# Kernel optimization log

Measured on AMD Instinct MI355X. Metric: run time of the kernel, lower is better.

The kernel has to match this reference:

```python
import jax, jax.numpy as jnp
import numpy as np

DIMS = (2000, 500, 400)
H, DK, DV = 8, 32, 32
DM = H * DV  # 256
NUM_CLASS = 5
BS = 16384
TEMP = DK ** 0.5
LN_EPS = 1e-6


def setup_inputs() -> dict:
    key = jax.random.key(0)
    ks = jax.random.split(key, 32)
    inp = {"input_data": jax.random.normal(ks[0], (BS, sum(DIMS)), dtype=jnp.float32)}
    i = 1
    for name, odim in (("q", H * DK), ("k", H * DK), ("v", H * DV)):
        for m, d in enumerate(DIMS):
            inp[f"w{name}{m}"] = jax.random.normal(ks[i], (d, odim), dtype=jnp.float32) * (1.0 / np.sqrt(d)); i += 1
            inp[f"b{name}{m}"] = jnp.zeros((odim,), dtype=jnp.float32)
    inp["fc_w"] = jax.random.normal(ks[i], (DM, DM), dtype=jnp.float32) * (1.0 / np.sqrt(DM)); i += 1
    inp["fc_b"] = jnp.zeros((DM,), dtype=jnp.float32)
    inp["ln_g"] = jnp.ones((DM,), dtype=jnp.float32)
    inp["ln_b"] = jnp.zeros((DM,), dtype=jnp.float32)
    inp["out_w"] = jax.random.normal(ks[i], (len(DIMS) * DM, NUM_CLASS), dtype=jnp.float32) * (1.0 / np.sqrt(len(DIMS) * DM)); i += 1
    inp["out_b"] = jnp.zeros((NUM_CLASS,), dtype=jnp.float32)
    return inp


def _forward(input_data, wq, bq, wk, bk, wv, bv, fc_w, fc_b, ln_g, ln_b, out_w, out_b):
    bs = input_data.shape[0]
    M = len(DIMS)
    offs = np.concatenate([[0], np.cumsum(DIMS)])
    xs = [input_data[:, offs[m]:offs[m + 1]] for m in range(M)]
    # per-modality projections -> [bs, M, H*D]
    q = jnp.stack([xs[m] @ wq[m] + bq[m] for m in range(M)], axis=1)
    k = jnp.stack([xs[m] @ wk[m] + bk[m] for m in range(M)], axis=1)
    v = jnp.stack([xs[m] @ wv[m] + bv[m] for m in range(M)], axis=1)
    # [bs, H, M, D]
    qh = q.reshape(bs, M, H, DK).transpose(0, 2, 1, 3)
    kh = k.reshape(bs, M, H, DK).transpose(0, 2, 1, 3)
    vh = v.reshape(bs, M, H, DV).transpose(0, 2, 1, 3)
    attn = jnp.einsum("bhmd,bhnd->bhmn", qh / TEMP, kh)
    attn = attn / jnp.abs(attn.min())  # global-min scaling as in source
    attn = attn / jnp.maximum(jnp.sum(jnp.abs(attn), axis=-1, keepdims=True), 1e-12)  # L1 normalize
    attn = jax.nn.softmax(attn, axis=-1)
    o = jnp.einsum("bhmn,bhnd->bhmd", attn, vh)
    o = o.transpose(0, 2, 1, 3).reshape(bs, M, DM)
    residual = v  # [bs, M, DM]
    o = o @ fc_w + fc_b
    x = o + residual
    mu = x.mean(axis=-1, keepdims=True)
    var = ((x - mu) ** 2).mean(axis=-1, keepdims=True)
    x = (x - mu) / jnp.sqrt(var + LN_EPS) * ln_g + ln_b
    return x.reshape(bs, -1) @ out_w + out_b


def reference(input_data, wq0, bq0, wq1, bq1, wq2, bq2, wk0, bk0, wk1, bk1, wk2, bk2,
              wv0, bv0, wv1, bv1, wv2, bv2, fc_w, fc_b, ln_g, ln_b, out_w, out_b):
    return _forward(input_data, (wq0, wq1, wq2), (bq0, bq1, bq2), (wk0, wk1, wk2), (bk0, bk1, bk2),
                    (wv0, wv1, wv2), (bv0, bv1, bv2), fc_w, fc_b, ln_g, ln_b, out_w, out_b)
```

## Files before the change

kernel.cpp:

```cpp
#include <hip/hip_runtime.h>
#include <hip/hip_bf16.h>

#define BATCH 16384
#define HEADS 8
#define DDK 32
#define NQKV 768
#define NCLASS 5
#define LN_EPS 1e-6f

#define BM 128
#define BN 128
#define BKK 32

typedef short bf16x8 __attribute__((ext_vector_type(8)));
typedef float f32x4 __attribute__((ext_vector_type(4)));

__device__ __forceinline__ unsigned short f2bf(float x) {
    unsigned u = __float_as_uint(x);
    u += 0x7fff + ((u >> 16) & 1);
    return (unsigned short)(u >> 16);
}
__device__ __forceinline__ float bf2f(unsigned short b) {
    return __uint_as_float(((unsigned)b) << 16);
}

__device__ __forceinline__ void gl16(const unsigned short* g, unsigned short* l) {
    __builtin_amdgcn_global_load_lds(
        (const __attribute__((address_space(1))) unsigned int*)g,
        (__attribute__((address_space(3))) unsigned int*)l, 16, 0, 0);
}

__global__ __launch_bounds__(256) void convert_x(const float* __restrict__ X,
                                                 unsigned short* __restrict__ A,
                                                 int Kdim, int Kpad, int xoff,
                                                 int r0, int nrows) {
    const int k8n = Kpad >> 3;
    const int total = nrows * k8n;
    for (int i = blockIdx.x * blockDim.x + threadIdx.x; i < total;
         i += gridDim.x * blockDim.x) {
        const int rl = i / k8n;
        const int k8 = (i - rl * k8n) << 3;
        const float* src = X + (size_t)(r0 + rl) * 2900 + xoff + k8;
        float xv[8];
        if (k8 + 8 <= Kdim) {
            float4 v0 = *reinterpret_cast<const float4*>(src);
            float4 v1 = *reinterpret_cast<const float4*>(src + 4);
            xv[0] = v0.x; xv[1] = v0.y; xv[2] = v0.z; xv[3] = v0.w;
            xv[4] = v1.x; xv[5] = v1.y; xv[6] = v1.z; xv[7] = v1.w;
        } else {
#pragma unroll
            for (int j = 0; j < 8; ++j) xv[j] = (k8 + j < Kdim) ? src[j] : 0.f;
        }
        union { unsigned short s[8]; uint4 v; } hi, lo;
#pragma unroll
        for (int j = 0; j < 8; ++j) {
            hi.s[j] = f2bf(xv[j]);
            lo.s[j] = f2bf(xv[j] - bf2f(hi.s[j]));
        }
        unsigned short* dst = A + (size_t)rl * (2 * Kpad) + k8;
        *reinterpret_cast<uint4*>(dst) = hi.v;
        *reinterpret_cast<uint4*>(dst + Kpad) = lo.v;
    }
}

__global__ __launch_bounds__(256) void convert_w(
    const float* __restrict__ wq, const float* __restrict__ wk,
    const float* __restrict__ wv, const float* __restrict__ bq,
    const float* __restrict__ bk, const float* __restrict__ bv,
    unsigned short* __restrict__ Bt, float* __restrict__ bias,
    int Kdim, int Kpad) {
    const int gid0 = blockIdx.x * blockDim.x + threadIdx.x;
    if (gid0 < NQKV) {
        const int p = gid0 >> 8, c = gid0 & 255;
        bias[gid0] = (p == 0 ? bq : p == 1 ? bk : bv)[c];
    }
    const int k8n = Kpad >> 3;
    const int total = NQKV * k8n;
    for (int i = gid0; i < total; i += gridDim.x * blockDim.x) {
        const int kb = i / NQKV;
        const int n = i - kb * NQKV;
        const int k8 = kb << 3;
        const int p = n >> 8, c = n & 255;
        const float* wsrc = (p == 0 ? wq : p == 1 ? wk : wv);
        union { unsigned short s[8]; uint4 v; } hi, lo;
#pragma unroll
        for (int j = 0; j < 8; ++j) {
            float x = (k8 + j < Kdim) ? wsrc[(size_t)(k8 + j) * 256 + c] : 0.f;
            hi.s[j] = f2bf(x);
            lo.s[j] = f2bf(x - bf2f(hi.s[j]));
        }
        unsigned short* dst = Bt + (size_t)n * (2 * Kpad) + k8;
        *reinterpret_cast<uint4*>(dst) = hi.v;
        *reinterpret_cast<uint4*>(dst + Kpad) = lo.v;
    }
}

__global__ __launch_bounds__(256) void qkv_mfma(
    const unsigned short* __restrict__ A,
    const unsigned short* __restrict__ Bt,
    const float* __restrict__ bias,
    float* __restrict__ Qo, float* __restrict__ Ko, float* __restrict__ Vo,
    int Kpad, int mz, int r0) {
    const int ld = 2 * Kpad;
    const int row0l = blockIdx.x * BM;
    const int nb = blockIdx.y * BN;
    const int tid = threadIdx.x;
    const int lane = tid & 63;
    const int w = tid >> 6;
    const int wr = w >> 1, wc = w & 1;

    __shared__ alignas(16) unsigned short AsH[BM * BKK];
    __shared__ alignas(16) unsigned short AsL[BM * BKK];
    __shared__ alignas(16) unsigned short BsH[BN * BKK];
    __shared__ alignas(16) unsigned short BsL[BN * BKK];

    f32x4 acc[4][4];
#pragma unroll
    for (int i = 0; i < 4; ++i)
#pragma unroll
        for (int j = 0; j < 4; ++j) acc[i][j] = (f32x4){0.f, 0.f, 0.f, 0.f};

    const int rs = lane >> 2;
    const int kk = (lane & 3) * 8;
    const size_t gA0 = (size_t)(row0l + w * 16 + rs) * ld + kk;
    const size_t gA1 = (size_t)(row0l + (w + 4) * 16 + rs) * ld + kk;
    const size_t gB0 = (size_t)(nb + w * 16 + rs) * ld + kk;
    const size_t gB1 = (size_t)(nb + (w + 4) * 16 + rs) * ld + kk;
    unsigned short* lAH0 = &AsH[w * 512];
    unsigned short* lAH1 = &AsH[(w + 4) * 512];
    unsigned short* lAL0 = &AsL[w * 512];
    unsigned short* lAL1 = &AsL[(w + 4) * 512];
    unsigned short* lBH0 = &BsH[w * 512];
    unsigned short* lBH1 = &BsH[(w + 4) * 512];
    unsigned short* lBL0 = &BsL[w * 512];
    unsigned short* lBL1 = &BsL[(w + 4) * 512];

    const int fr = lane & 15;
    const int fk = (lane >> 4) * 8;
    const int aoff0 = (wr * 64 + fr) * BKK + fk;
    const int boff0 = (wc * 64 + fr) * BKK + fk;

    const int nk = Kpad >> 5;
#pragma unroll 1
    for (int kt = 0; kt < nk; ++kt) {
        const int k0 = kt * BKK;
        __syncthreads();
        gl16(A + gA0 + k0, lAH0);
        gl16(A + gA1 + k0, lAH1);
        gl16(A + Kpad + gA0 + k0, lAL0);
        gl16(A + Kpad + gA1 + k0, lAL1);
        gl16(Bt + gB0 + k0, lBH0);
        gl16(Bt + gB1 + k0, lBH1);
        gl16(Bt + Kpad + gB0 + k0, lBL0);
        gl16(Bt + Kpad + gB1 + k0, lBL1);
        __syncthreads();

        bf16x8 ah[4], bh[4];
#pragma unroll
        for (int mi = 0; mi < 4; ++mi)
            ah[mi] = *reinterpret_cast<const bf16x8*>(&AsH[aoff0 + mi * 16 * BKK]);
#pragma unroll
        for (int ni = 0; ni < 4; ++ni)
            bh[ni] = *reinterpret_cast<const bf16x8*>(&BsH[boff0 + ni * 16 * BKK]);
#pragma unroll
        for (int mi = 0; mi < 4; ++mi)
#pragma unroll
            for (int ni = 0; ni < 4; ++ni)
                acc[mi][ni] = __builtin_amdgcn_mfma_f32_16x16x32_bf16(
                    ah[mi], bh[ni], acc[mi][ni], 0, 0, 0);
        {
            bf16x8 al[4];
#pragma unroll
            for (int mi = 0; mi < 4; ++mi)
                al[mi] = *reinterpret_cast<const bf16x8*>(&AsL[aoff0 + mi * 16 * BKK]);
#pragma unroll
            for (int mi = 0; mi < 4; ++mi)
#pragma unroll
                for (int ni = 0; ni < 4; ++ni)
                    acc[mi][ni] = __builtin_amdgcn_mfma_f32_16x16x32_bf16(
                        al[mi], bh[ni], acc[mi][ni], 0, 0, 0);
        }
        {
            bf16x8 bl[4];
#pragma unroll
            for (int ni = 0; ni < 4; ++ni)
                bl[ni] = *reinterpret_cast<const bf16x8*>(&BsL[boff0 + ni * 16 * BKK]);
#pragma unroll
            for (int mi = 0; mi < 4; ++mi)
#pragma unroll
                for (int ni = 0; ni < 4; ++ni)
                    acc[mi][ni] = __builtin_amdgcn_mfma_f32_16x16x32_bf16(
                        ah[mi], bl[ni], acc[mi][ni], 0, 0, 0);
        }
    }

#pragma unroll
    for (int ni = 0; ni < 4; ++ni) {
        const int gc = nb + wc * 64 + ni * 16 + fr;
        const int proj = gc >> 8;
        const int col = gc & 255;
        const float bv = bias[gc];
        float* outp = (proj == 0 ? Qo : proj == 1 ? Ko : Vo);
#pragma unroll
        for (int mi = 0; mi < 4; ++mi) {
            const int gr = r0 + row0l + wr * 64 + mi * 16 + (lane >> 4) * 4;
            float* p = outp + (size_t)gr * NQKV + mz * 256 + col;
#pragma unroll
            for (int j = 0; j < 4; ++j)
                p[(size_t)j * NQKV] = acc[mi][ni][j] + bv;
        }
    }
}

__global__ __launch_bounds__(256) void attn_kernel(const float* __restrict__ Q,
                                                   const float* __restrict__ K,
                                                   const float* __restrict__ V,
                                                   float* __restrict__ O) {
    const int s = blockIdx.x;
    const int t = threadIdx.x;
    __shared__ float qs[NQKV], ks[NQKV], vs[NQKV];
    __shared__ float att[HEADS][3][3];

    const size_t base = (size_t)s * NQKV;
    for (int i = t; i < NQKV; i += 256) {
        qs[i] = Q[base + i];
        ks[i] = K[base + i];
        vs[i] = V[base + i];
    }
    __syncthreads();

    if (t < 72) {
        const int h = t / 9, ij = t % 9, i = ij / 3, j = ij % 3;
        const float* qp = &qs[i * 256 + h * 32];
        const float* kp = &ks[j * 256 + h * 32];
        float sc = 0.f;
#pragma unroll
        for (int d = 0; d < DDK; ++d) sc = fmaf(qp[d], kp[d], sc);
        att[h][i][j] = sc;
    }
    __syncthreads();
    if (t < 24) {
        const int h = t / 3, i = t % 3;
        float s0 = att[h][i][0], s1 = att[h][i][1], s2 = att[h][i][2];
        float r = fabsf(s0) + fabsf(s1) + fabsf(s2);
        r = fmaxf(r, 1e-12f);
        float p0 = s0 / r, p1 = s1 / r, p2 = s2 / r;
        float mx = fmaxf(p0, fmaxf(p1, p2));
        float e0 = expf(p0 - mx), e1 = expf(p1 - mx), e2 = expf(p2 - mx);
        float inv = 1.f / (e0 + e1 + e2);
        att[h][i][0] = e0 * inv;
        att[h][i][1] = e1 * inv;
        att[h][i][2] = e2 * inv;
    }
    __syncthreads();

    const int c = t;
    const int h = c >> 5;
#pragma unroll
    for (int m = 0; m < 3; ++m) {
        float o = att[h][m][0] * vs[c] + att[h][m][1] * vs[256 + c] + att[h][m][2] * vs[512 + c];
        O[base + m * 256 + c] = o;
    }
}

__global__ __launch_bounds__(256) void fc_gemm(const float* __restrict__ A,
                                               const float* __restrict__ W,
                                               const float* __restrict__ bias,
                                               const float* __restrict__ resid,
                                               float* __restrict__ X) {
    const int row0 = blockIdx.x * BM;
    const int nbase = blockIdx.y * BN;

    __shared__ float As[BKK][BM + 4];
    __shared__ float Bs[BKK][BN + 4];

    const int tid = threadIdx.x;
    const int tx = tid & 15;
    const int ty = tid >> 4;

    float acc[8][8];
#pragma unroll
    for (int i = 0; i < 8; ++i)
#pragma unroll
        for (int j = 0; j < 8; ++j) acc[i][j] = 0.f;

    for (int k0 = 0; k0 < 256; k0 += BKK) {
        {
            const int r = tid >> 3;
            const int kq = (tid & 7) * 4;
#pragma unroll
            for (int it = 0; it < 4; ++it) {
                const int row = r + it * 32;
                float4 v = *reinterpret_cast<const float4*>(
                    &A[(size_t)(row0 + row) * 256 + k0 + kq]);
                As[kq + 0][row] = v.x;
                As[kq + 1][row] = v.y;
                As[kq + 2][row] = v.z;
                As[kq + 3][row] = v.w;
            }
        }
        {
            const int kkk = tid >> 5;
            const int n4 = (tid & 31) * 4;
#pragma unroll
            for (int it = 0; it < 4; ++it) {
                const int krow = kkk + it * 8;
                *reinterpret_cast<float4*>(&Bs[krow][n4]) =
                    *reinterpret_cast<const float4*>(&W[(size_t)(k0 + krow) * 256 + nbase + n4]);
            }
        }
        __syncthreads();
#pragma unroll 8
        for (int k = 0; k < BKK; ++k) {
            float4 a0 = *reinterpret_cast<float4*>(&As[k][ty * 4]);
            float4 a1 = *reinterpret_cast<float4*>(&As[k][ty * 4 + 64]);
            float4 b0 = *reinterpret_cast<float4*>(&Bs[k][tx * 4]);
            float4 b1 = *reinterpret_cast<float4*>(&Bs[k][tx * 4 + 64]);
            float av[8] = {a0.x, a0.y, a0.z, a0.w, a1.x, a1.y, a1.z, a1.w};
            float bv[8] = {b0.x, b0.y, b0.z, b0.w, b1.x, b1.y, b1.z, b1.w};
#pragma unroll
            for (int i = 0; i < 8; ++i)
#pragma unroll
                for (int j = 0; j < 8; ++j)
                    acc[i][j] = fmaf(av[i], bv[j], acc[i][j]);
        }
        __syncthreads();
    }

#pragma unroll
    for (int rh = 0; rh < 2; ++rh) {
#pragma unroll
        for (int i = 0; i < 4; ++i) {
            const int row = row0 + rh * 64 + ty * 4 + i;
#pragma unroll
            for (int ch = 0; ch < 2; ++ch) {
                const int c = ch * 64 + tx * 4;
                const size_t off = (size_t)row * 256 + nbase + c;
                float4 rv = *reinterpret_cast<const float4*>(&resid[off]);
                float4 o;
                o.x = acc[rh * 4 + i][ch * 4 + 0] + bias[nbase + c + 0] + rv.x;
                o.y = acc[rh * 4 + i][ch * 4 + 1] + bias[nbase + c + 1] + rv.y;
                o.z = acc[rh * 4 + i][ch * 4 + 2] + bias[nbase + c + 2] + rv.z;
                o.w = acc[rh * 4 + i][ch * 4 + 3] + bias[nbase + c + 3] + rv.w;
                *reinterpret_cast<float4*>(&X[off]) = o;
            }
        }
    }
}

__global__ __launch_bounds__(256) void ln_out_kernel(const float* __restrict__ X,
                                                     const float* __restrict__ g,
                                                     const float* __restrict__ bb,
                                                     const float* __restrict__ ow,
                                                     const float* __restrict__ ob,
                                                     float* __restrict__ out) {
    const int s = blockIdx.x;
    const int t = threadIdx.x;
    const int lane = t & 63, wv = t >> 6;
    __shared__ float xr[NQKV];
    __shared__ float red1[4], red2[4];
    __shared__ float cpart[4][NCLASS];

    const size_t base = (size_t)s * NQKV;
    const float gg = g[t];
    const float bbv = bb[t];

    for (int m = 0; m < 3; ++m) {
        float v = X[base + m * 256 + t];
        float s1 = v, s2 = v * v;
#pragma unroll
        for (int off = 32; off > 0; off >>= 1) {
            s1 += __shfl_down(s1, off);
            s2 += __shfl_down(s2, off);
        }
        if (lane == 0) { red1[wv] = s1; red2[wv] = s2; }
        __syncthreads();
        const float tot = red1[0] + red1[1] + red1[2] + red1[3];
        const float tot2 = red2[0] + red2[1] + red2[2] + red2[3];
        const float mu = tot * (1.f / 256.f);
        const float var = tot2 * (1.f / 256.f) - mu * mu;
        const float inv = 1.0f / sqrtf(var + LN_EPS);
        xr[m * 256 + t] = (v - mu) * inv * gg + bbv;
        __syncthreads();
    }

    float p[NCLASS] = {0.f, 0.f, 0.f, 0.f, 0.f};
    for (int i = t; i < NQKV; i += 256) {
        const float xv = xr[i];
#pragma unroll
        for (int c = 0; c < NCLASS; ++c) p[c] = fmaf(xv, ow[i * NCLASS + c], p[c]);
    }
#pragma unroll
    for (int c = 0; c < NCLASS; ++c) {
        float pv = p[c];
#pragma unroll
        for (int off = 32; off > 0; off >>= 1) pv += __shfl_down(pv, off);
        if (lane == 0) cpart[wv][c] = pv;
    }
    __syncthreads();
    if (t < NCLASS)
        out[(size_t)s * NCLASS + t] =
            cpart[0][t] + cpart[1][t] + cpart[2][t] + cpart[3][t] + ob[t];
}

extern "C" void kernel_launch(void* const* d_in, const int* in_sizes, int n_in,
                              void* d_out, int out_size, void* d_ws, size_t ws_size,
                              hipStream_t stream) {
    const float* x = (const float*)d_in[0];
    const float* wq[3] = {(const float*)d_in[1], (const float*)d_in[3], (const float*)d_in[5]};
    const float* bq[3] = {(const float*)d_in[2], (const float*)d_in[4], (const float*)d_in[6]};
    const float* wk[3] = {(const float*)d_in[7], (const float*)d_in[9], (const float*)d_in[11]};
    const float* bk[3] = {(const float*)d_in[8], (const float*)d_in[10], (const float*)d_in[12]};
    const float* wvv[3] = {(const float*)d_in[13], (const float*)d_in[15], (const float*)d_in[17]};
    const float* bv[3] = {(const float*)d_in[14], (const float*)d_in[16], (const float*)d_in[18]};
    const float* fc_w = (const float*)d_in[19];
    const float* fc_b = (const float*)d_in[20];
    const float* ln_g = (const float*)d_in[21];
    const float* ln_b = (const float*)d_in[22];
    const float* out_w = (const float*)d_in[23];
    const float* out_b = (const float*)d_in[24];

    float* ws = (float*)d_ws;
    const size_t SZ = (size_t)BATCH * NQKV;
    float* Q = ws;
    float* Kb = ws + SZ;
    float* Vb = ws + 2 * SZ;
    float* biasx = ws + 3 * SZ;
    unsigned short* Bt = (unsigned short*)(biasx + NQKV);
    unsigned short* Aext = Bt + (size_t)NQKV * 4096;

    const size_t fixed_bytes = (3 * SZ + NQKV) * sizeof(float) +
                               (size_t)NQKV * 4096 * sizeof(unsigned short);
    size_t avail = (ws_size > fixed_bytes) ? ws_size - fixed_bytes : 0;
    size_t rc = (avail / (4096 * sizeof(unsigned short))) & ~(size_t)127;
    if (rc < 128) rc = 128;
    if (rc > BATCH) rc = BATCH;
    const int rows_chunk = (int)rc;

    float* O = Kb;
    float* X = Q;

    const int Kdim[3] = {2000, 500, 400};
    const int Kpad[3] = {2048, 512, 448};
    const int xoff[3] = {0, 2000, 2500};

    for (int m = 0; m < 3; ++m) {
        convert_w<<<768, 256, 0, stream>>>(wq[m], wk[m], wvv[m], bq[m], bk[m], bv[m],
                                           Bt, biasx, Kdim[m], Kpad[m]);
        for (int r0 = 0; r0 < BATCH; r0 += rows_chunk) {
            const int nr = (BATCH - r0 < rows_chunk) ? (BATCH - r0) : rows_chunk;
            const int cgrid = ((nr * (Kpad[m] >> 3)) + 255) / 256;
            convert_x<<<(cgrid < 2048 ? cgrid : 2048), 256, 0, stream>>>(
                x, Aext, Kdim[m], Kpad[m], xoff[m], r0, nr);
            dim3 g(nr / BM, NQKV / BN);
            qkv_mfma<<<g, 256, 0, stream>>>(Aext, Bt, biasx, Q, Kb, Vb, Kpad[m], m, r0);
        }
    }

    attn_kernel<<<BATCH, 256, 0, stream>>>(Q, Kb, Vb, O);

    dim3 g3((BATCH * 3) / BM, 2);
    fc_gemm<<<g3, 256, 0, stream>>>(O, fc_w, fc_b, Vb, X);

    ln_out_kernel<<<BATCH, 256, 0, stream>>>(X, ln_g, ln_b, out_w, out_b, (float*)d_out);
}
```

Baseline: 804.3 us.

## Switch split-precision GEMMs to fp16 with single-term weights and MFMA fc layer

Replaces the bf16 hi/lo three-product emulation in the QKV GEMM with fp16: activations stay split into hi/lo, but weights are rounded to a single fp16 term. This removes one third of the MFMA work and one of the LDS tile loads per K step. The scalar fp32 fc GEMM becomes an fp16 MFMA kernel whose attention output is split into hi/lo halves. Weight conversion for all three modalities and the fc layer is merged into one launch, and row chunks are sized per modality. The risk is accuracy: fp16 weights carry only 11 bits of mantissa, and fp16 range could overflow.

```diff
diff --git a/kernel.cpp b/kernel.cpp
--- a/kernel.cpp
+++ b/kernel.cpp
@@ -12,26 +12,17 @@
 #define BN 128
 #define BKK 32
 
-typedef short bf16x8 __attribute__((ext_vector_type(8)));
+typedef _Float16 f16x8 __attribute__((ext_vector_type(8)));
 typedef float f32x4 __attribute__((ext_vector_type(4)));
 
-__device__ __forceinline__ unsigned short f2bf(float x) {
-    unsigned u = __float_as_uint(x);
-    u += 0x7fff + ((u >> 16) & 1);
-    return (unsigned short)(u >> 16);
-}
-__device__ __forceinline__ float bf2f(unsigned short b) {
-    return __uint_as_float(((unsigned)b) << 16);
-}
-
-__device__ __forceinline__ void gl16(const unsigned short* g, unsigned short* l) {
+__device__ __forceinline__ void gl16(const void* g, void* l) {
     __builtin_amdgcn_global_load_lds(
         (const __attribute__((address_space(1))) unsigned int*)g,
         (__attribute__((address_space(3))) unsigned int*)l, 16, 0, 0);
 }
 
 __global__ __launch_bounds__(256) void convert_x(const float* __restrict__ X,
-                                                 unsigned short* __restrict__ A,
+                                                 _Float16* __restrict__ A,
                                                  int Kdim, int Kpad, int xoff,
                                                  int r0, int nrows) {
     const int k8n = Kpad >> 3;
@@ -51,53 +42,71 @@
 #pragma unroll
             for (int j = 0; j < 8; ++j) xv[j] = (k8 + j < Kdim) ? src[j] : 0.f;
         }
-        union { unsigned short s[8]; uint4 v; } hi, lo;
+        union { _Float16 h[8]; uint4 v; } hi, lo;
 #pragma unroll
         for (int j = 0; j < 8; ++j) {
-            hi.s[j] = f2bf(xv[j]);
-            lo.s[j] = f2bf(xv[j] - bf2f(hi.s[j]));
-        }
-        unsigned short* dst = A + (size_t)rl * (2 * Kpad) + k8;
+            hi.h[j] = (_Float16)xv[j];
+            lo.h[j] = (_Float16)(xv[j] - (float)hi.h[j]);
+        }
+        _Float16* dst = A + (size_t)rl * (2 * Kpad) + k8;
         *reinterpret_cast<uint4*>(dst) = hi.v;
         *reinterpret_cast<uint4*>(dst + Kpad) = lo.v;
     }
 }
 
-__global__ __launch_bounds__(256) void convert_w(
-    const float* __restrict__ wq, const float* __restrict__ wk,
-    const float* __restrict__ wv, const float* __restrict__ bq,
-    const float* __restrict__ bk, const float* __restrict__ bv,
-    unsigned short* __restrict__ Bt, float* __restrict__ bias,
-    int Kdim, int Kpad) {
-    const int gid0 = blockIdx.x * blockDim.x + threadIdx.x;
-    if (gid0 < NQKV) {
-        const int p = gid0 >> 8, c = gid0 & 255;
-        bias[gid0] = (p == 0 ? bq : p == 1 ? bk : bv)[c];
-    }
-    const int k8n = Kpad >> 3;
-    const int total = NQKV * k8n;
-    for (int i = gid0; i < total; i += gridDim.x * blockDim.x) {
-        const int kb = i / NQKV;
-        const int n = i - kb * NQKV;
-        const int k8 = kb << 3;
-        const int p = n >> 8, c = n & 255;
-        const float* wsrc = (p == 0 ? wq : p == 1 ? wk : wv);
-        union { unsigned short s[8]; uint4 v; } hi, lo;
-#pragma unroll
-        for (int j = 0; j < 8; ++j) {
-            float x = (k8 + j < Kdim) ? wsrc[(size_t)(k8 + j) * 256 + c] : 0.f;
-            hi.s[j] = f2bf(x);
-            lo.s[j] = f2bf(x - bf2f(hi.s[j]));
-        }
-        unsigned short* dst = Bt + (size_t)n * (2 * Kpad) + k8;
-        *reinterpret_cast<uint4*>(dst) = hi.v;
-        *reinterpret_cast<uint4*>(dst + Kpad) = lo.v;
+struct WArgs {
+    const float* w[3][3];
+    const float* b[3][3];
+    const float* fcw;
+    _Float16* Bt;
+    float* biasx;
+    _Float16* fcWh;
+};
+
+__global__ __launch_bounds__(256) void convert_w_all(WArgs a) {
+    const int y = blockIdx.y;
+    const int gid = blockIdx.x * 256 + threadIdx.x;
+    if (y < 3) {
+        const int m = y;
+        const int Kdim = (m == 0) ? 2000 : (m == 1 ? 500 : 400);
+        const int Kpad = (m == 0) ? 2048 : (m == 1 ? 512 : 448);
+        if (gid < NQKV) {
+            const int p = gid >> 8, c = gid & 255;
+            a.biasx[m * NQKV + gid] = a.b[p][m][c];
+        }
+        const int k8n = Kpad >> 3;
+        const int total = NQKV * k8n;
+        _Float16* dst0 = a.Bt + (size_t)m * NQKV * 2048;
+        for (int i = gid; i < total; i += gridDim.x * 256) {
+            const int kb = i / NQKV;
+            const int n = i - kb * NQKV;
+            const int k8 = kb << 3;
+            const int p = n >> 8, c = n & 255;
+            const float* wsrc = a.w[p][m];
+            union { _Float16 h[8]; uint4 v; } hi;
+#pragma unroll
+            for (int j = 0; j < 8; ++j) {
+                float x = (k8 + j < Kdim) ? wsrc[(size_t)(k8 + j) * 256 + c] : 0.f;
+                hi.h[j] = (_Float16)x;
+            }
+            *reinterpret_cast<uint4*>(dst0 + (size_t)n * Kpad + k8) = hi.v;
+        }
+    } else {
+        for (int i = gid; i < 256 * 32; i += gridDim.x * 256) {
+            const int n = i & 255;
+            const int k8 = (i >> 8) << 3;
+            union { _Float16 h[8]; uint4 v; } hi;
+#pragma unroll
+            for (int j = 0; j < 8; ++j)
+                hi.h[j] = (_Float16)a.fcw[(size_t)(k8 + j) * 256 + n];
+            *reinterpret_cast<uint4*>(a.fcWh + (size_t)n * 256 + k8) = hi.v;
+        }
     }
 }
 
 __global__ __launch_bounds__(256) void qkv_mfma(
-    const unsigned short* __restrict__ A,
-    const unsigned short* __restrict__ Bt,
+    const _Float16* __restrict__ A,
+    const _Float16* __restrict__ Bt,
     const float* __restrict__ bias,
     float* __restrict__ Qo, float* __restrict__ Ko, float* __restrict__ Vo,
     int Kpad, int mz, int r0) {
@@ -109,10 +118,9 @@
     const int w = tid >> 6;
     const int wr = w >> 1, wc = w & 1;
 
-    __shared__ alignas(16) unsigned short AsH[BM * BKK];
-    __shared__ alignas(16) unsigned short AsL[BM * BKK];
-    __shared__ alignas(16) unsigned short BsH[BN * BKK];
-    __shared__ alignas(16) unsigned short BsL[BN * BKK];
+    __shared__ alignas(16) _Float16 AsH[BM * BKK];
+    __shared__ alignas(16) _Float16 AsL[BM * BKK];
+    __shared__ alignas(16) _Float16 BsH[BN * BKK];
 
     f32x4 acc[4][4];
 #pragma unroll
@@ -124,16 +132,14 @@
     const int kk = (lane & 3) * 8;
     const size_t gA0 = (size_t)(row0l + w * 16 + rs) * ld + kk;
     const size_t gA1 = (size_t)(row0l + (w + 4) * 16 + rs) * ld + kk;
-    const size_t gB0 = (size_t)(nb + w * 16 + rs) * ld + kk;
-    const size_t gB1 = (size_t)(nb + (w + 4) * 16 + rs) * ld + kk;
-    unsigned short* lAH0 = &AsH[w * 512];
-    unsigned short* lAH1 = &AsH[(w + 4) * 512];
-    unsigned short* lAL0 = &AsL[w * 512];
-    unsigned short* lAL1 = &AsL[(w + 4) * 512];
-    unsigned short* lBH0 = &BsH[w * 512];
-    unsigned short* lBH1 = &BsH[(w + 4) * 512];
-    unsigned short* lBL0 = &BsL[w * 512];
-    unsigned short* lBL1 = &BsL[(w + 4) * 512];
+    const size_t gB0 = (size_t)(nb + w * 16 + rs) * Kpad + kk;
+    const size_t gB1 = (size_t)(nb + (w + 4) * 16 + rs) * Kpad + kk;
+    _Float16* lAH0 = &AsH[w * 512];
+    _Float16* lAH1 = &AsH[(w + 4) * 512];
+    _Float16* lAL0 = &AsL[w * 512];
+    _Float16* lAL1 = &AsL[(w + 4) * 512];
+    _Float16* lBH0 = &BsH[w * 512];
+    _Float16* lBH1 = &BsH[(w + 4) * 512];
 
     const int fr = lane & 15;
     const int fk = (lane >> 4) * 8;
@@ -151,46 +157,32 @@
         gl16(A + Kpad + gA1 + k0, lAL1);
         gl16(Bt + gB0 + k0, lBH0);
         gl16(Bt + gB1 + k0, lBH1);
-        gl16(Bt + Kpad + gB0 + k0, lBL0);
-        gl16(Bt + Kpad + gB1 + k0, lBL1);
-        __syncthreads();
-
-        bf16x8 ah[4], bh[4];
+        __syncthreads();
+
+        f16x8 ah[4], bh[4];
 #pragma unroll
         for (int mi = 0; mi < 4; ++mi)
-            ah[mi] = *reinterpret_cast<const bf16x8*>(&AsH[aoff0 + mi * 16 * BKK]);
+            ah[mi] = *reinterpret_cast<const f16x8*>(&AsH[aoff0 + mi * 16 * BKK]);
 #pragma unroll
         for (int ni = 0; ni < 4; ++ni)
-            bh[ni] = *reinterpret_cast<const bf16x8*>(&BsH[boff0 + ni * 16 * BKK]);
+            bh[ni] = *reinterpret_cast<const f16x8*>(&BsH[boff0 + ni * 16 * BKK]);
 #pragma unroll
         for (int mi = 0; mi < 4; ++mi)
 #pragma unroll
             for (int ni = 0; ni < 4; ++ni)
-                acc[mi][ni] = __builtin_amdgcn_mfma_f32_16x16x32_bf16(
+                acc[mi][ni] = __builtin_amdgcn_mfma_f32_16x16x32_f16(
                     ah[mi], bh[ni], acc[mi][ni], 0, 0, 0);
         {
-            bf16x8 al[4];
+            f16x8 al[4];
 #pragma unroll
             for (int mi = 0; mi < 4; ++mi)
-                al[mi] = *reinterpret_cast<const bf16x8*>(&AsL[aoff0 + mi * 16 * BKK]);
+                al[mi] = *reinterpret_cast<const f16x8*>(&AsL[aoff0 + mi * 16 * BKK]);
 #pragma unroll
             for (int mi = 0; mi < 4; ++mi)
 #pragma unroll
                 for (int ni = 0; ni < 4; ++ni)
-                    acc[mi][ni] = __builtin_amdgcn_mfma_f32_16x16x32_bf16(
+                    acc[mi][ni] = __builtin_amdgcn_mfma_f32_16x16x32_f16(
                         al[mi], bh[ni], acc[mi][ni], 0, 0, 0);
-        }
-        {
-            bf16x8 bl[4];
-#pragma unroll
-            for (int ni = 0; ni < 4; ++ni)
-                bl[ni] = *reinterpret_cast<const bf16x8*>(&BsL[boff0 + ni * 16 * BKK]);
-#pragma unroll
-            for (int mi = 0; mi < 4; ++mi)
-#pragma unroll
-                for (int ni = 0; ni < 4; ++ni)
-                    acc[mi][ni] = __builtin_amdgcn_mfma_f32_16x16x32_bf16(
-                        ah[mi], bl[ni], acc[mi][ni], 0, 0, 0);
         }
     }
 
@@ -215,7 +207,7 @@
 __global__ __launch_bounds__(256) void attn_kernel(const float* __restrict__ Q,
                                                    const float* __restrict__ K,
                                                    const float* __restrict__ V,
-                                                   float* __restrict__ O) {
+                                                   _Float16* __restrict__ Of) {
     const int s = blockIdx.x;
     const int t = threadIdx.x;
     __shared__ float qs[NQKV], ks[NQKV], vs[NQKV];
@@ -259,90 +251,103 @@
 #pragma unroll
     for (int m = 0; m < 3; ++m) {
         float o = att[h][m][0] * vs[c] + att[h][m][1] * vs[256 + c] + att[h][m][2] * vs[512 + c];
-        O[base + m * 256 + c] = o;
-    }
-}
-
-__global__ __launch_bounds__(256) void fc_gemm(const float* __restrict__ A,
-                                               const float* __restrict__ W,
-                                               const float* __restrict__ bias,
+        const size_t ob = ((size_t)s * 3 + m) * 512 + c;
+        _Float16 oh = (_Float16)o;
+        Of[ob] = oh;
+        Of[ob + 256] = (_Float16)(o - (float)oh);
+    }
+}
+
+__global__ __launch_bounds__(256) void fc_mfma(const _Float16* __restrict__ O,
+                                               const _Float16* __restrict__ Wh,
+                                               const float* __restrict__ fcb,
                                                const float* __restrict__ resid,
                                                float* __restrict__ X) {
     const int row0 = blockIdx.x * BM;
-    const int nbase = blockIdx.y * BN;
-
-    __shared__ float As[BKK][BM + 4];
-    __shared__ float Bs[BKK][BN + 4];
-
+    const int nb = blockIdx.y * BN;
     const int tid = threadIdx.x;
-    const int tx = tid & 15;
-    const int ty = tid >> 4;
-
-    float acc[8][8];
-#pragma unroll
-    for (int i = 0; i < 8; ++i)
-#pragma unroll
-        for (int j = 0; j < 8; ++j) acc[i][j] = 0.f;
-
-    for (int k0 = 0; k0 < 256; k0 += BKK) {
+    const int lane = tid & 63;
+    const int w = tid >> 6;
+    const int wr = w >> 1, wc = w & 1;
+
+    __shared__ alignas(16) _Float16 AsH[BM * BKK];
+    __shared__ alignas(16) _Float16 AsL[BM * BKK];
+    __shared__ alignas(16) _Float16 BsH[BN * BKK];
+
+    f32x4 acc[4][4];
+#pragma unroll
+    for (int i = 0; i < 4; ++i)
+#pragma unroll
+        for (int j = 0; j < 4; ++j) acc[i][j] = (f32x4){0.f, 0.f, 0.f, 0.f};
+
+    const int rs = lane >> 2;
+    const int kk = (lane & 3) * 8;
+    const size_t gA0 = (size_t)(row0 + w * 16 + rs) * 512 + kk;
+    const size_t gA1 = (size_t)(row0 + (w + 4) * 16 + rs) * 512 + kk;
+    const size_t gB0 = (size_t)(nb + w * 16 + rs) * 256 + kk;
+    const size_t gB1 = (size_t)(nb + (w + 4) * 16 + rs) * 256 + kk;
+    _Float16* lAH0 = &AsH[w * 512];
+    _Float16* lAH1 = &AsH[(w + 4) * 512];
+    _Float16* lAL0 = &AsL[w * 512];
+    _Float16* lAL1 = &AsL[(w + 4) * 512];
+    _Float16* lBH0 = &BsH[w * 512];
+    _Float16* lBH1 = &BsH[(w + 4) * 512];
+
+    const int fr = lane & 15;
+    const int fk = (lane >> 4) * 8;
+    const int aoff0 = (wr * 64 + fr) * BKK + fk;
+    const int boff0 = (wc * 64 + fr) * BKK + fk;
+
+#pragma unroll 1
+    for (int kt = 0; kt < 8; ++kt) {
+        const int k0 = kt * BKK;
+        __syncthreads();
+        gl16(O + gA0 + k0, lAH0);
+        gl16(O + gA1 + k0, lAH1);
+        gl16(O + 256 + gA0 + k0, lAL0);
+        gl16(O + 256 + gA1 + k0, lAL1);
+        gl16(Wh + gB0 + k0, lBH0);
+        gl16(Wh + gB1 + k0, lBH1);
+        __syncthreads();
+
+        f16x8 ah[4], bh[4];
+#pragma unroll
+        for (int mi = 0; mi < 4; ++mi)
+            ah[mi] = *reinterpret_cast<const f16x8*>(&AsH[aoff0 + mi * 16 * BKK]);
+#pragma unroll
+        for (int ni = 0; ni < 4; ++ni)
+            bh[ni] = *reinterpret_cast<const f16x8*>(&BsH[boff0 + ni * 16 * BKK]);
+#pragma unroll
+        for (int mi = 0; mi < 4; ++mi)
+#pragma unroll
+            for (int ni = 0; ni < 4; ++ni)
+                acc[mi][ni] = __builtin_amdgcn_mfma_f32_16x16x32_f16(
+                    ah[mi], bh[ni], acc[mi][ni], 0, 0, 0);
         {
-            const int r = tid >> 3;
-            const int kq = (tid & 7) * 4;
-#pragma unroll
-            for (int it = 0; it < 4; ++it) {
-                const int row = r + it * 32;
-                float4 v = *reinterpret_cast<const float4*>(
-                    &A[(size_t)(row0 + row) * 256 + k0 + kq]);
-                As[kq + 0][row] = v.x;
-                As[kq + 1][row] = v.y;
-                As[kq + 2][row] = v.z;
-                As[kq + 3][row] = v.w;
-            }
-        }
-        {
-            const int kkk = tid >> 5;
-            const int n4 = (tid & 31) * 4;
-#pragma unroll
-            for (int it = 0; it < 4; ++it) {
-                const int krow = kkk + it * 8;
-                *reinterpret_cast<float4*>(&Bs[krow][n4]) =
-                    *reinterpret_cast<const float4*>(&W[(size_t)(k0 + krow) * 256 + nbase + n4]);
-            }
-        }
-        __syncthreads();
-#pragma unroll 8
-        for (int k = 0; k < BKK; ++k) {
-            float4 a0 = *reinterpret_cast<float4*>(&As[k][ty * 4]);
-            float4 a1 = *reinterpret_cast<float4*>(&As[k][ty * 4 + 64]);
-            float4 b0 = *reinterpret_cast<float4*>(&Bs[k][tx * 4]);
-            float4 b1 = *reinterpret_cast<float4*>(&Bs[k][tx * 4 + 64]);
-            float av[8] = {a0.x, a0.y, a0.z, a0.w, a1.x, a1.y, a1.z, a1.w};
-            float bv[8] = {b0.x, b0.y, b0.z, b0.w, b1.x, b1.y, b1.z, b1.w};
-#pragma unroll
-            for (int i = 0; i < 8; ++i)
-#pragma unroll
-                for (int j = 0; j < 8; ++j)
-                    acc[i][j] = fmaf(av[i], bv[j], acc[i][j]);
-        }
-        __syncthreads();
-    }
-
-#pragma unroll
-    for (int rh = 0; rh < 2; ++rh) {
-#pragma unroll
-        for (int i = 0; i < 4; ++i) {
-            const int row = row0 + rh * 64 + ty * 4 + i;
-#pragma unroll
-            for (int ch = 0; ch < 2; ++ch) {
-                const int c = ch * 64 + tx * 4;
-                const size_t off = (size_t)row * 256 + nbase + c;
-                float4 rv = *reinterpret_cast<const float4*>(&resid[off]);
-                float4 o;
-                o.x = acc[rh * 4 + i][ch * 4 + 0] + bias[nbase + c + 0] + rv.x;
-                o.y = acc[rh * 4 + i][ch * 4 + 1] + bias[nbase + c + 1] + rv.y;
-                o.z = acc[rh * 4 + i][ch * 4 + 2] + bias[nbase + c + 2] + rv.z;
-                o.w = acc[rh * 4 + i][ch * 4 + 3] + bias[nbase + c + 3] + rv.w;
-                *reinterpret_cast<float4*>(&X[off]) = o;
+            f16x8 al[4];
+#pragma unroll
+            for (int mi = 0; mi < 4; ++mi)
+                al[mi] = *reinterpret_cast<const f16x8*>(&AsL[aoff0 + mi * 16 * BKK]);
+#pragma unroll
+            for (int mi = 0; mi < 4; ++mi)
+#pragma unroll
+                for (int ni = 0; ni < 4; ++ni)
+                    acc[mi][ni] = __builtin_amdgcn_mfma_f32_16x16x32_f16(
+                        al[mi], bh[ni], acc[mi][ni], 0, 0, 0);
+        }
+    }
+
+#pragma unroll
+    for (int ni = 0; ni < 4; ++ni) {
+        const int gc = nb + wc * 64 + ni * 16 + fr;
+        const float bv = fcb[gc];
+#pragma unroll
+        for (int mi = 0; mi < 4; ++mi) {
+            const int gr = row0 + wr * 64 + mi * 16 + (lane >> 4) * 4;
+#pragma unroll
+            for (int j = 0; j < 4; ++j) {
+                const size_t off = (size_t)(gr + j) * 256 + gc;
+                X[off] = acc[mi][ni][j] + bv + resid[off];
             }
         }
     }
@@ -407,12 +412,13 @@
                               void* d_out, int out_size, void* d_ws, size_t ws_size,
                               hipStream_t stream) {
     const float* x = (const float*)d_in[0];
-    const float* wq[3] = {(const float*)d_in[1], (const float*)d_in[3], (const float*)d_in[5]};
-    const float* bq[3] = {(const float*)d_in[2], (const float*)d_in[4], (const float*)d_in[6]};
-    const float* wk[3] = {(const float*)d_in[7], (const float*)d_in[9], (const float*)d_in[11]};
-    const float* bk[3] = {(const float*)d_in[8], (const float*)d_in[10], (const float*)d_in[12]};
-    const float* wvv[3] = {(const float*)d_in[13], (const float*)d_in[15], (const float*)d_in[17]};
-    const float* bv[3] = {(const float*)d_in[14], (const float*)d_in[16], (const float*)d_in[18]};
+    WArgs wa;
+    int idx = 1;
+    for (int p = 0; p < 3; ++p)
+        for (int m = 0; m < 3; ++m) {
+            wa.w[p][m] = (const float*)d_in[idx++];
+            wa.b[p][m] = (const float*)d_in[idx++];
+        }
     const float* fc_w = (const float*)d_in[19];
     const float* fc_b = (const float*)d_in[20];
     const float* ln_g = (const float*)d_in[21];
@@ -426,41 +432,44 @@
     float* Kb = ws + SZ;
     float* Vb = ws + 2 * SZ;
     float* biasx = ws + 3 * SZ;
-    unsigned short* Bt = (unsigned short*)(biasx + NQKV);
-    unsigned short* Aext = Bt + (size_t)NQKV * 4096;
-
-    const size_t fixed_bytes = (3 * SZ + NQKV) * sizeof(float) +
-                               (size_t)NQKV * 4096 * sizeof(unsigned short);
-    size_t avail = (ws_size > fixed_bytes) ? ws_size - fixed_bytes : 0;
-    size_t rc = (avail / (4096 * sizeof(unsigned short))) & ~(size_t)127;
-    if (rc < 128) rc = 128;
-    if (rc > BATCH) rc = BATCH;
-    const int rows_chunk = (int)rc;
-
-    float* O = Kb;
+    _Float16* Bt = (_Float16*)(biasx + 3 * NQKV);
+    _Float16* fcWh = Bt + (size_t)3 * NQKV * 2048;
+    _Float16* pool = fcWh + 256 * 256;
+
+    wa.fcw = fc_w; wa.Bt = Bt; wa.biasx = biasx; wa.fcWh = fcWh;
+
+    const size_t fixed_bytes = (size_t)((char*)pool - (char*)d_ws);
+    const size_t avail = (ws_size > fixed_bytes) ? ws_size - fixed_bytes : 0;
+
     float* X = Q;
+    _Float16* Of = pool;
 
     const int Kdim[3] = {2000, 500, 400};
     const int Kpad[3] = {2048, 512, 448};
     const int xoff[3] = {0, 2000, 2500};
 
+    convert_w_all<<<dim3(768, 4), 256, 0, stream>>>(wa);
+
     for (int m = 0; m < 3; ++m) {
-        convert_w<<<768, 256, 0, stream>>>(wq[m], wk[m], wvv[m], bq[m], bk[m], bv[m],
-                                           Bt, biasx, Kdim[m], Kpad[m]);
+        size_t rc = (avail / ((size_t)4 * Kpad[m])) & ~(size_t)127;
+        if (rc < 128) rc = 128;
+        if (rc > BATCH) rc = BATCH;
+        const int rows_chunk = (int)rc;
         for (int r0 = 0; r0 < BATCH; r0 += rows_chunk) {
             const int nr = (BATCH - r0 < rows_chunk) ? (BATCH - r0) : rows_chunk;
             const int cgrid = ((nr * (Kpad[m] >> 3)) + 255) / 256;
             convert_x<<<(cgrid < 2048 ? cgrid : 2048), 256, 0, stream>>>(
-                x, Aext, Kdim[m], Kpad[m], xoff[m], r0, nr);
+                x, pool, Kdim[m], Kpad[m], xoff[m], r0, nr);
             dim3 g(nr / BM, NQKV / BN);
-            qkv_mfma<<<g, 256, 0, stream>>>(Aext, Bt, biasx, Q, Kb, Vb, Kpad[m], m, r0);
-        }
-    }
-
-    attn_kernel<<<BATCH, 256, 0, stream>>>(Q, Kb, Vb, O);
-
-    dim3 g3((BATCH * 3) / BM, 2);
-    fc_gemm<<<g3, 256, 0, stream>>>(O, fc_w, fc_b, Vb, X);
+            qkv_mfma<<<g, 256, 0, stream>>>(pool, Bt + (size_t)m * NQKV * 2048,
+                                            biasx + m * NQKV, Q, Kb, Vb,
+                                            Kpad[m], m, r0);
+        }
+    }
+
+    attn_kernel<<<BATCH, 256, 0, stream>>>(Q, Kb, Vb, Of);
+
+    fc_mfma<<<dim3((BATCH * 3) / BM, 2), 256, 0, stream>>>(Of, fcWh, fc_b, Vb, X);
 
     ln_out_kernel<<<BATCH, 256, 0, stream>>>(X, ln_g, ln_b, out_w, out_b, (float*)d_out);
 }
```

Result: faster. 733.7 us (-8.8%).
